# Optimization experiments

Hardware: AMD Instinct MI355X
Metric: run time of the kernel (lower is better)

Reference implementation:

```python
import jax, jax.numpy as jnp
import numpy as np

N, E, C = 100000, 500000, 128
LN_EPS = 1e-5


def setup_inputs() -> dict:
    key = jax.random.key(0)
    ks = jax.random.split(key, 6)
    x = jax.random.normal(ks[0], (N, C), dtype=jnp.float32)
    edge_index = jax.random.randint(ks[1], (2, E), 0, N, dtype=jnp.int32)
    edge_weight = jax.random.uniform(ks[2], (E,), dtype=jnp.float32)
    scale = 1.0 / np.sqrt(C)
    W1 = jax.random.normal(ks[3], (C, C), dtype=jnp.float32) * scale
    W2 = jax.random.normal(ks[4], (C, C), dtype=jnp.float32) * scale
    b1 = jnp.zeros((C,), jnp.float32)
    b2 = jnp.zeros((C,), jnp.float32)
    g1 = jnp.ones((C,), jnp.float32)
    g2 = jnp.ones((C,), jnp.float32)
    beta1 = jnp.zeros((C,), jnp.float32)
    beta2 = jnp.zeros((C,), jnp.float32)
    return {"x": x, "edge_index": edge_index, "edge_weight": edge_weight,
            "W1": W1, "b1": b1, "g1": g1, "beta1": beta1,
            "W2": W2, "b2": b2, "g2": g2, "beta2": beta2}


def _gcn_norm(edge_index, edge_weight, n):
    # add self loops (weight 1.0), then symmetric deg^{-1/2} normalization;
    # degree() in the source counts edges into col (unweighted), incl. self loops
    src = jnp.concatenate([edge_index[0], jnp.arange(n, dtype=edge_index.dtype)])
    dst = jnp.concatenate([edge_index[1], jnp.arange(n, dtype=edge_index.dtype)])
    ew = jnp.concatenate([edge_weight, jnp.ones((n,), edge_weight.dtype)])
    deg = jax.ops.segment_sum(jnp.ones_like(ew), dst, num_segments=n)
    dis = jnp.where(deg > 0, jax.lax.rsqrt(jnp.maximum(deg, 1.0)) * (deg > 0), 0.0)
    w = dis[src] * ew * dis[dst]
    return src, dst, w


def _layernorm(y, g, b):
    mu = jnp.mean(y, axis=-1, keepdims=True)
    var = jnp.mean(jnp.square(y - mu), axis=-1, keepdims=True)
    return (y - mu) * jax.lax.rsqrt(var + LN_EPS) * g + b


def _gcn_layer(x, W, bias, src, dst, w, n):
    h = x @ W                               # [N,C] linear (no bias)
    msg = w[:, None] * h[src]               # gather + edge scaling [E+N,C]
    out = jax.ops.segment_sum(msg, dst, num_segments=n)  # scatter-add
    return out + bias


def reference(x, edge_index, edge_weight, W1, b1, g1, beta1, W2, b2, g2, beta2):
    n = x.shape[0]
    src, dst, w = _gcn_norm(edge_index, edge_weight, n)
    identity = x
    h = _gcn_layer(x, W1, b1, src, dst, w, n)
    h = jax.nn.gelu(_layernorm(h, g1, beta1), approximate=False)
    h = _gcn_layer(h, W2, b2, src, dst, w, n)
    h = jax.nn.gelu(_layernorm(h, g2, beta2), approximate=False)
    return h + identity
```

## Files before the change

### kernel.cpp

```cpp
#include <hip/hip_runtime.h>
#include <math.h>

#define C 128
#define CAPF 1024
#define DSTRIDE 132

typedef __attribute__((ext_vector_type(8))) short short8;
typedef __attribute__((ext_vector_type(4))) float f32x4;
typedef __attribute__((ext_vector_type(2))) float f32x2;
typedef __attribute__((ext_vector_type(8))) unsigned short ushort8_t;

__device__ inline unsigned short f2b(float f) {
    union { float f; unsigned int u; } v; v.f = f;
    unsigned int u = v.u;
    return (unsigned short)((u + 0x7FFFu + ((u >> 16) & 1u)) >> 16);
}
__device__ inline float bits2f(unsigned int u) {
    union { unsigned int u; float f; } v; v.u = u; return v.f;
}

__device__ inline void acc8(f32x2* a, uint4 u, f32x2 s) {
    f32x2 v0 = {bits2f(u.x << 16), bits2f(u.x & 0xFFFF0000u)};
    f32x2 v1 = {bits2f(u.y << 16), bits2f(u.y & 0xFFFF0000u)};
    f32x2 v2 = {bits2f(u.z << 16), bits2f(u.z & 0xFFFF0000u)};
    f32x2 v3 = {bits2f(u.w << 16), bits2f(u.w & 0xFFFF0000u)};
    a[0] += s * v0;
    a[1] += s * v1;
    a[2] += s * v2;
    a[3] += s * v3;
}

__device__ inline void agg_row_only(
    int row, int c0, int kbeg, int kend, int eb0,
    const int2* __restrict__ eds, const int2* __restrict__ edata,
    const unsigned short* __restrict__ Hb, const float* __restrict__ dis, f32x2* a) {
    {
        float d = dis[row];
        f32x2 d2 = {d * d, d * d};
        uint4 hu = *(const uint4*)(Hb + (size_t)row * C + c0);
        acc8(a, hu, d2);
    }
    const int kc = kend < CAPF ? kend : CAPF;
    int k = kbeg;
    for (; k + 3 < kc; k += 4) {
        int2 e0 = eds[k];
        int2 e1 = eds[k + 1];
        int2 e2 = eds[k + 2];
        int2 e3 = eds[k + 3];
        uint4 u0 = *(const uint4*)(Hb + (size_t)e0.x * C + c0);
        uint4 u1 = *(const uint4*)(Hb + (size_t)e1.x * C + c0);
        uint4 u2 = *(const uint4*)(Hb + (size_t)e2.x * C + c0);
        uint4 u3 = *(const uint4*)(Hb + (size_t)e3.x * C + c0);
        float w0 = bits2f((unsigned int)e0.y);
        float w1 = bits2f((unsigned int)e1.y);
        float w2 = bits2f((unsigned int)e2.y);
        float w3 = bits2f((unsigned int)e3.y);
        acc8(a, u0, f32x2{w0, w0});
        acc8(a, u1, f32x2{w1, w1});
        acc8(a, u2, f32x2{w2, w2});
        acc8(a, u3, f32x2{w3, w3});
    }
    for (; k < kc; ++k) {
        int2 e0 = eds[k];
        uint4 u0 = *(const uint4*)(Hb + (size_t)e0.x * C + c0);
        float w0 = bits2f((unsigned int)e0.y);
        acc8(a, u0, f32x2{w0, w0});
    }
    for (; k < kend; ++k) {
        int2 e0 = edata[eb0 + k];
        uint4 u0 = *(const uint4*)(Hb + (size_t)e0.x * C + c0);
        float w0 = bits2f((unsigned int)e0.y);
        acc8(a, u0, f32x2{w0, w0});
    }
}


__global__ void k_cnt_cvt(const int* __restrict__ dst, int* __restrict__ cnt, int e, int bc,
                          const float* __restrict__ x, unsigned short* __restrict__ xb,
                          int ncvt8) {
    const int bid = blockIdx.x;
    const int tid = threadIdx.x;
    if (bid < bc) {
        int i = bid * 256 + tid;
        if (i < ncvt8) {
            const float4* xp = (const float4*)(x + (size_t)i * 8);
            float4 v0 = xp[0];
            float4 v1 = xp[1];
            ushort8_t pkt;
            pkt[0] = f2b(v0.x); pkt[1] = f2b(v0.y); pkt[2] = f2b(v0.z); pkt[3] = f2b(v0.w);
            pkt[4] = f2b(v1.x); pkt[5] = f2b(v1.y); pkt[6] = f2b(v1.z); pkt[7] = f2b(v1.w);
            *(ushort8_t*)(xb + (size_t)i * 8) = pkt;
        }
    } else {
        int i = (bid - bc) * 256 + tid;
        if (i < e) atomicAdd(&cnt[dst[i]], 1);
    }
}

__global__ __launch_bounds__(256) void k_scan_a(const int* __restrict__ cnt,
                                                int* __restrict__ rowbeg,
                                                int* __restrict__ blocksum,
                                                float* __restrict__ dis, int n) {
    const int tid = threadIdx.x;
    const int i = blockIdx.x * 256 + tid;
    const int lane = tid & 63, wv = tid >> 6;
    int v = (i < n) ? cnt[i] : 0;
    int x = v;
    #pragma unroll
    for (int off = 1; off < 64; off <<= 1) {
        int y = __shfl_up(x, off, 64);
        if (lane >= off) x += y;
    }
    __shared__ int wsum[4];
    if (lane == 63) wsum[wv] = x;
    __syncthreads();
    int woff = 0;
    #pragma unroll
    for (int k = 0; k < 4; ++k) if (k < wv) woff += wsum[k];
    int incl = x + woff;
    if (i < n) {
        rowbeg[i] = incl - v;
        dis[i] = rsqrtf((float)v + 1.0f);
    }
    if (tid == 255) blocksum[blockIdx.x] = incl;
}

__global__ __launch_bounds__(512) void k_scan_b_pack(int* __restrict__ bs, int nb,
    const float* __restrict__ W1, const float* __restrict__ W2,
    unsigned short* __restrict__ W1p, unsigned short* __restrict__ W2p) {
    const int tid = threadIdx.x;
    if (blockIdx.x == 0) {
        __shared__ int s[512];
        int v = (tid < nb) ? bs[tid] : 0;
        s[tid] = v;
        __syncthreads();
        for (int off = 1; off < 512; off <<= 1) {
            int t = 0;
            if (tid >= off) t = s[tid - off];
            __syncthreads();
            s[tid] += t;
            __syncthreads();
        }
        if (tid < nb) bs[tid] = s[tid] - v;
    } else {
        int idx = (blockIdx.x - 1) * 512 + tid;
        const float* W = (idx < C * C) ? W1 : W2;
        unsigned short* Wp = (idx < C * C) ? W1p : W2p;
        int p = idx & (C * C - 1);
        int j = p & 7;
        int l = (p >> 3) & 63;
        int t = p >> 9;
        int ks = t & 3, ct = t >> 2;
        int k = ks * 32 + ((l >> 4) << 3) + j;
        int c = (ct << 4) + (l & 15);
        Wp[p] = f2b(W[k * C + c]);
    }
}

__global__ void k_scan_c(const int* __restrict__ cnt, const int* __restrict__ bs,
                         int* __restrict__ rowbeg, int* __restrict__ rowcur, int n) {
    int i = blockIdx.x * blockDim.x + threadIdx.x;
    if (i >= n) return;
    int rb = rowbeg[i] + bs[i >> 8];
    rowbeg[i] = rb;
    rowcur[i] = rb;
    if (i == n - 1) rowbeg[n] = rb + cnt[i];
}

__global__ void k_place(const int* __restrict__ src, const int* __restrict__ dst,
                        const float* __restrict__ ew, const float* __restrict__ dis,
                        int* __restrict__ rowcur, int2* __restrict__ edata, int e) {
    int i = blockIdx.x * blockDim.x + threadIdx.x;
    if (i >= e) return;
    int s = src[i], d = dst[i];
    int p = atomicAdd(&rowcur[d], 1);
    float w = dis[s] * ew[i] * dis[d];
    union { float f; int i; } wb; wb.f = w;
    edata[p] = make_int2(s, wb.i);
}

__global__ __launch_bounds__(512) void k_layer(
    const int* __restrict__ rowbeg, const int2* __restrict__ edata,
    const unsigned short* __restrict__ Xin, const float* __restrict__ dis,
    const unsigned short* __restrict__ Wp,
    const float* __restrict__ bias, const float* __restrict__ g,
    const float* __restrict__ beta,
    const unsigned short* __restrict__ xb_resid,
    unsigned short* __restrict__ out_bf16, float* __restrict__ out_f32, int n) {
    __shared__ int2 eds[CAPF];
    __shared__ unsigned short xs[32 * C];
    __shared__ float dacc[32 * DSTRIDE];
    const int tid = threadIdx.x;
    const int lane = tid & 63;
    const int wid = tid >> 6;
    const int grp = lane >> 4;
    const int sub = lane & 15;
    const int base = blockIdx.x * 32;
    const int c0 = sub * 8;

    const int eb0 = rowbeg[base];
    const int top = (base + 32 < n) ? base + 32 : n;
    const int len = rowbeg[top] - eb0;
    const int lcap = len < CAPF ? len : CAPF;
    for (int i = tid; i < lcap; i += 512) eds[i] = edata[eb0 + i];
    __syncthreads();

    {
        int r = wid * 4 + grp;
        int row = base + r;
        f32x2 a[4] = {f32x2{0.f, 0.f}, f32x2{0.f, 0.f}, f32x2{0.f, 0.f}, f32x2{0.f, 0.f}};
        if (row < n) {
            int kbeg = rowbeg[row] - eb0;
            int kend = rowbeg[row + 1] - eb0;
            agg_row_only(row, c0, kbeg, kend, eb0, eds, edata, Xin, dis, a);
        }
        ushort8_t pkt;
        #pragma unroll
        for (int q = 0; q < 4; ++q) { pkt[q * 2] = f2b(a[q].x); pkt[q * 2 + 1] = f2b(a[q].y); }
        int byte = (r * 256 + c0 * 2) ^ ((r & 7) << 4);
        *(ushort8_t*)((char*)xs + byte) = pkt;
    }
    __syncthreads();

    {
        const int wm = wid >> 2;
        const int wn = wid & 3;
        const int arow = wm * 16 + (lane & 15);
        const int kg = lane >> 4;

        f32x4 acc[2] = {f32x4{0, 0, 0, 0}, f32x4{0, 0, 0, 0}};

        #pragma unroll
        for (int ks = 0; ks < 4; ++ks) {
            int abyte = (arow * 256 + ks * 64 + kg * 16) ^ ((arow & 7) << 4);
            short8 av = *(const short8*)((const char*)xs + abyte);
            #pragma unroll
            for (int nt = 0; nt < 2; ++nt) {
                int ct = wn * 2 + nt;
                short8 bv = *(const short8*)(Wp + (size_t)((ct * 4 + ks) * 64 + lane) * 8);
                acc[nt] = __builtin_amdgcn_mfma_f32_16x16x32_bf16(av, bv, acc[nt], 0, 0, 0);
            }
        }

        const int rb = wm * 16 + kg * 4;
        #pragma unroll
        for (int nt = 0; nt < 2; ++nt) {
            int col = wn * 32 + nt * 16 + (lane & 15);
            float bv = bias[col];
            #pragma unroll
            for (int r2 = 0; r2 < 4; ++r2)
                dacc[(rb + r2) * DSTRIDE + col] = acc[nt][r2] + bv;
        }
    }
    __syncthreads();

    {
        int r = wid * 4 + grp;
        int row = base + r;
        if (row >= n) return;

        const float* dp = dacc + r * DSTRIDE + c0;
        float4 v0 = *(const float4*)(dp);
        float4 v1 = *(const float4*)(dp + 4);
        float a[8] = {v0.x, v0.y, v0.z, v0.w, v1.x, v1.y, v1.z, v1.w};

        float s = 0.f, sq = 0.f;
        #pragma unroll
        for (int j = 0; j < 8; ++j) { s += a[j]; sq += a[j] * a[j]; }
        #pragma unroll
        for (int off = 8; off >= 1; off >>= 1) {
            s  += __shfl_xor(s, off, 64);
            sq += __shfl_xor(sq, off, 64);
        }
        float mu = s * (1.0f / C);
        float var = sq * (1.0f / C) - mu * mu;
        float rstd = rsqrtf(var + 1e-5f);

        float4 gv0 = *(const float4*)(g + c0);
        float4 gv1 = *(const float4*)(g + c0 + 4);
        float4 be0 = *(const float4*)(beta + c0);
        float4 be1 = *(const float4*)(beta + c0 + 4);
        float gg[8] = {gv0.x, gv0.y, gv0.z, gv0.w, gv1.x, gv1.y, gv1.z, gv1.w};
        float bb[8] = {be0.x, be0.y, be0.z, be0.w, be1.x, be1.y, be1.z, be1.w};

        float t[8];
        #pragma unroll
        for (int j = 0; j < 8; ++j) {
            float v = (a[j] - mu) * rstd * gg[j] + bb[j];
            t[j] = 0.5f * v * (1.0f + erff(v * 0.70710678118654752f));
        }

        if (out_f32 != nullptr) {
            ushort8_t rv = *(const ushort8_t*)(xb_resid + (size_t)row * C + c0);
            #pragma unroll
            for (int j = 0; j < 8; ++j)
                t[j] += bits2f(((unsigned int)(unsigned short)rv[j]) << 16);
            *(float4*)(out_f32 + (size_t)row * C + c0) = make_float4(t[0], t[1], t[2], t[3]);
            *(float4*)(out_f32 + (size_t)row * C + c0 + 4) = make_float4(t[4], t[5], t[6], t[7]);
        } else {
            ushort8_t pkt;
            #pragma unroll
            for (int j = 0; j < 8; ++j) pkt[j] = f2b(t[j]);
            *(ushort8_t*)(out_bf16 + (size_t)row * C + c0) = pkt;
        }
    }
}


extern "C" void kernel_launch(void* const* d_in, const int* in_sizes, int n_in,
                              void* d_out, int out_size, void* d_ws, size_t ws_size,
                              hipStream_t stream) {
    const float* x      = (const float*)d_in[0];
    const int*   eidx   = (const int*)d_in[1];
    const float* ew     = (const float*)d_in[2];
    const float* W1     = (const float*)d_in[3];
    const float* b1     = (const float*)d_in[4];
    const float* g1     = (const float*)d_in[5];
    const float* beta1  = (const float*)d_in[6];
    const float* W2     = (const float*)d_in[7];
    const float* b2     = (const float*)d_in[8];
    const float* g2     = (const float*)d_in[9];
    const float* beta2  = (const float*)d_in[10];

    const int n = in_sizes[0] / C;
    const int e = in_sizes[2];
    const int* src = eidx;
    const int* dst = eidx + e;

    float* out = (float*)d_out;

    char* p = (char*)d_ws;
    auto alloc = [&](size_t bytes) {
        char* q = p;
        p += (bytes + 255) & ~(size_t)255;
        return q;
    };
    float* dis      = (float*)alloc(sizeof(float) * n);
    int*   cnt      = (int*)alloc(sizeof(int) * n);
    int*   rowbeg   = (int*)alloc(sizeof(int) * (n + 1));
    int*   rowcur   = (int*)alloc(sizeof(int) * n);
    int*   blocksum = (int*)alloc(sizeof(int) * 512);
    int2*  edata    = (int2*)alloc(sizeof(int2) * e);
    unsigned short* xb    = (unsigned short*)alloc(sizeof(unsigned short) * (size_t)n * C);
    unsigned short* hact1 = (unsigned short*)alloc(sizeof(unsigned short) * (size_t)n * C);
    unsigned short* W1p   = (unsigned short*)alloc(sizeof(unsigned short) * C * C);
    unsigned short* W2p   = (unsigned short*)alloc(sizeof(unsigned short) * C * C);

    const int B = 256;
    const int gn = (n + B - 1) / B;
    const int ge = (e + B - 1) / B;
    const int ncvt8 = n * C / 8;
    const int bc = (ncvt8 + B - 1) / B;

    hipMemsetAsync(cnt, 0, sizeof(int) * n, stream);
    k_cnt_cvt<<<bc + ge, B, 0, stream>>>(dst, cnt, e, bc, x, xb, ncvt8);
    k_scan_a<<<gn, B, 0, stream>>>(cnt, rowbeg, blocksum, dis, n);
    k_scan_b_pack<<<1 + (2 * C * C) / 512, 512, 0, stream>>>(blocksum, gn, W1, W2, W1p, W2p);
    k_scan_c<<<gn, B, 0, stream>>>(cnt, blocksum, rowbeg, rowcur, n);
    k_place<<<ge, B, 0, stream>>>(src, dst, ew, dis, rowcur, edata, e);

    k_layer<<<(n + 31) / 32, 512, 0, stream>>>(rowbeg, edata, xb, dis, W1p,
                                               b1, g1, beta1, nullptr,
                                               hact1, nullptr, n);

    k_layer<<<(n + 31) / 32, 512, 0, stream>>>(rowbeg, edata, hact1, dis, W2p,
                                               b2, g2, beta2, xb,
                                               nullptr, out, n);
}
```

Measured before the change: 155.7 us.

## Replace three-pass prefix scan with single-pass atomic segment allocation

Merges the block scan, block-sum scan and offset fix-up kernels into one kernel, which also packs the weights. Each 256-row block reserves its CSR segment by doing an atomicAdd on a global cursor, so segments are contiguous within a block but appear in arbitrary order across blocks. Row ends are now computed as rowbeg plus cnt instead of from rowbeg[row+1], so k_layer takes cnt as an extra input. This removes two kernel launches and their serial dependencies, at the cost of a non-monotonic edge layout across blocks and one extra cnt read per row.

```diff
diff --git a/kernel.cpp b/kernel.cpp
--- a/kernel.cpp
+++ b/kernel.cpp
@@ -97,53 +97,14 @@
     }
 }
 
-__global__ __launch_bounds__(256) void k_scan_a(const int* __restrict__ cnt,
-                                                int* __restrict__ rowbeg,
-                                                int* __restrict__ blocksum,
-                                                float* __restrict__ dis, int n) {
-    const int tid = threadIdx.x;
-    const int i = blockIdx.x * 256 + tid;
-    const int lane = tid & 63, wv = tid >> 6;
-    int v = (i < n) ? cnt[i] : 0;
-    int x = v;
-    #pragma unroll
-    for (int off = 1; off < 64; off <<= 1) {
-        int y = __shfl_up(x, off, 64);
-        if (lane >= off) x += y;
-    }
-    __shared__ int wsum[4];
-    if (lane == 63) wsum[wv] = x;
-    __syncthreads();
-    int woff = 0;
-    #pragma unroll
-    for (int k = 0; k < 4; ++k) if (k < wv) woff += wsum[k];
-    int incl = x + woff;
-    if (i < n) {
-        rowbeg[i] = incl - v;
-        dis[i] = rsqrtf((float)v + 1.0f);
-    }
-    if (tid == 255) blocksum[blockIdx.x] = incl;
-}
-
-__global__ __launch_bounds__(512) void k_scan_b_pack(int* __restrict__ bs, int nb,
+__global__ __launch_bounds__(256) void k_scan_apack(
+    const int* __restrict__ cnt, int* __restrict__ rowbeg, int* __restrict__ rowcur,
+    float* __restrict__ dis, int* __restrict__ cursor, int n, int gn,
     const float* __restrict__ W1, const float* __restrict__ W2,
     unsigned short* __restrict__ W1p, unsigned short* __restrict__ W2p) {
     const int tid = threadIdx.x;
-    if (blockIdx.x == 0) {
-        __shared__ int s[512];
-        int v = (tid < nb) ? bs[tid] : 0;
-        s[tid] = v;
-        __syncthreads();
-        for (int off = 1; off < 512; off <<= 1) {
-            int t = 0;
-            if (tid >= off) t = s[tid - off];
-            __syncthreads();
-            s[tid] += t;
-            __syncthreads();
-        }
-        if (tid < nb) bs[tid] = s[tid] - v;
-    } else {
-        int idx = (blockIdx.x - 1) * 512 + tid;
+    if (blockIdx.x >= gn) {
+        int idx = (blockIdx.x - gn) * 256 + tid;
         const float* W = (idx < C * C) ? W1 : W2;
         unsigned short* Wp = (idx < C * C) ? W1p : W2p;
         int p = idx & (C * C - 1);
@@ -154,17 +115,33 @@
         int k = ks * 32 + ((l >> 4) << 3) + j;
         int c = (ct << 4) + (l & 15);
         Wp[p] = f2b(W[k * C + c]);
-    }
-}
-
-__global__ void k_scan_c(const int* __restrict__ cnt, const int* __restrict__ bs,
-                         int* __restrict__ rowbeg, int* __restrict__ rowcur, int n) {
-    int i = blockIdx.x * blockDim.x + threadIdx.x;
-    if (i >= n) return;
-    int rb = rowbeg[i] + bs[i >> 8];
-    rowbeg[i] = rb;
-    rowcur[i] = rb;
-    if (i == n - 1) rowbeg[n] = rb + cnt[i];
+        return;
+    }
+    const int i = blockIdx.x * 256 + tid;
+    const int lane = tid & 63, wv = tid >> 6;
+    int v = (i < n) ? cnt[i] : 0;
+    int x = v;
+    #pragma unroll
+    for (int off = 1; off < 64; off <<= 1) {
+        int y = __shfl_up(x, off, 64);
+        if (lane >= off) x += y;
+    }
+    __shared__ int wsum[4];
+    __shared__ int gbase;
+    if (lane == 63) wsum[wv] = x;
+    __syncthreads();
+    int woff = 0;
+    #pragma unroll
+    for (int k = 0; k < 4; ++k) if (k < wv) woff += wsum[k];
+    int incl = x + woff;
+    if (tid == 255) gbase = atomicAdd(cursor, incl);
+    __syncthreads();
+    if (i < n) {
+        int rb = gbase + incl - v;
+        rowbeg[i] = rb;
+        rowcur[i] = rb;
+        dis[i] = rsqrtf((float)v + 1.0f);
+    }
 }
 
 __global__ void k_place(const int* __restrict__ src, const int* __restrict__ dst,
@@ -180,7 +157,8 @@
 }
 
 __global__ __launch_bounds__(512) void k_layer(
-    const int* __restrict__ rowbeg, const int2* __restrict__ edata,
+    const int* __restrict__ rowbeg, const int* __restrict__ cnt,
+    const int2* __restrict__ edata,
     const unsigned short* __restrict__ Xin, const float* __restrict__ dis,
     const unsigned short* __restrict__ Wp,
     const float* __restrict__ bias, const float* __restrict__ g,
@@ -199,8 +177,9 @@
     const int c0 = sub * 8;
 
     const int eb0 = rowbeg[base];
-    const int top = (base + 32 < n) ? base + 32 : n;
-    const int len = rowbeg[top] - eb0;
+    int last = base + 31;
+    if (last >= n) last = n - 1;
+    const int len = rowbeg[last] + cnt[last] - eb0;
     const int lcap = len < CAPF ? len : CAPF;
     for (int i = tid; i < lcap; i += 512) eds[i] = edata[eb0 + i];
     __syncthreads();
@@ -211,7 +190,7 @@
         f32x2 a[4] = {f32x2{0.f, 0.f}, f32x2{0.f, 0.f}, f32x2{0.f, 0.f}, f32x2{0.f, 0.f}};
         if (row < n) {
             int kbeg = rowbeg[row] - eb0;
-            int kend = rowbeg[row + 1] - eb0;
+            int kend = kbeg + cnt[row];
             agg_row_only(row, c0, kbeg, kend, eb0, eds, edata, Xin, dis, a);
         }
         ushort8_t pkt;
@@ -336,34 +315,34 @@
         return q;
     };
     float* dis      = (float*)alloc(sizeof(float) * n);
-    int*   cnt      = (int*)alloc(sizeof(int) * n);
-    int*   rowbeg   = (int*)alloc(sizeof(int) * (n + 1));
+    int*   cnt      = (int*)alloc(sizeof(int) * (n + 1));
+    int*   rowbeg   = (int*)alloc(sizeof(int) * n);
     int*   rowcur   = (int*)alloc(sizeof(int) * n);
-    int*   blocksum = (int*)alloc(sizeof(int) * 512);
     int2*  edata    = (int2*)alloc(sizeof(int2) * e);
     unsigned short* xb    = (unsigned short*)alloc(sizeof(unsigned short) * (size_t)n * C);
     unsigned short* hact1 = (unsigned short*)alloc(sizeof(unsigned short) * (size_t)n * C);
     unsigned short* W1p   = (unsigned short*)alloc(sizeof(unsigned short) * C * C);
     unsigned short* W2p   = (unsigned short*)alloc(sizeof(unsigned short) * C * C);
+    int* cursor = cnt + n;
 
     const int B = 256;
     const int gn = (n + B - 1) / B;
     const int ge = (e + B - 1) / B;
     const int ncvt8 = n * C / 8;
     const int bc = (ncvt8 + B - 1) / B;
-
-    hipMemsetAsync(cnt, 0, sizeof(int) * n, stream);
+    const int packb = (2 * C * C) / B;
+
+    hipMemsetAsync(cnt, 0, sizeof(int) * (n + 1), stream);
     k_cnt_cvt<<<bc + ge, B, 0, stream>>>(dst, cnt, e, bc, x, xb, ncvt8);
-    k_scan_a<<<gn, B, 0, stream>>>(cnt, rowbeg, blocksum, dis, n);
-    k_scan_b_pack<<<1 + (2 * C * C) / 512, 512, 0, stream>>>(blocksum, gn, W1, W2, W1p, W2p);
-    k_scan_c<<<gn, B, 0, stream>>>(cnt, blocksum, rowbeg, rowcur, n);
+    k_scan_apack<<<gn + packb, B, 0, stream>>>(cnt, rowbeg, rowcur, dis, cursor, n, gn,
+                                               W1, W2, W1p, W2p);
     k_place<<<ge, B, 0, stream>>>(src, dst, ew, dis, rowcur, edata, e);
 
-    k_layer<<<(n + 31) / 32, 512, 0, stream>>>(rowbeg, edata, xb, dis, W1p,
+    k_layer<<<(n + 31) / 32, 512, 0, stream>>>(rowbeg, cnt, edata, xb, dis, W1p,
                                                b1, g1, beta1, nullptr,
                                                hact1, nullptr, n);
 
-    k_layer<<<(n + 31) / 32, 512, 0, stream>>>(rowbeg, edata, hact1, dis, W2p,
+    k_layer<<<(n + 31) / 32, 512, 0, stream>>>(rowbeg, cnt, edata, hact1, dis, W2p,
                                                b2, g2, beta2, xb,
                                                nullptr, out, n);
 }
```

New measurement: 159.4 us. +2.4%, slower.
